# Kernel optimization log

Hardware: AMD Instinct MI355X
Metric: run time of the kernel (lower is better)

Reference implementation:

```python
import jax, jax.numpy as jnp
import numpy as np

B, L, D, H = 2, 2048, 1024, 16
DH = D // H  # 64
SIGMA = float(np.sqrt(DH))  # sigma=None, learnable_sigma=False -> sqrt(d_head)


def setup_inputs() -> dict:
    key = jax.random.key(0)
    ks = jax.random.split(key, 5)
    x = jax.random.normal(ks[0], (B, L, D), dtype=jnp.float32)
    # causal visibility mask (1 = visible, 0 = masked), [B,1,L,L]
    mask = jnp.broadcast_to(jnp.tril(jnp.ones((L, L), jnp.int32))[None, None], (B, 1, L, L))
    scale = 0.02
    W_q = jax.random.normal(ks[1], (D, D), dtype=jnp.float32) * scale
    W_k = jax.random.normal(ks[2], (D, D), dtype=jnp.float32) * scale
    W_v = jax.random.normal(ks[3], (D, D), dtype=jnp.float32) * scale
    W_o = jax.random.normal(ks[4], (D, D), dtype=jnp.float32) * scale
    return {"x": x, "mask": mask, "W_q": W_q, "W_k": W_k, "W_v": W_v, "W_o": W_o}


def _split_heads(t):
    # [B,L,D] -> [B,H,L,DH]
    b, l, _ = t.shape
    return t.reshape(b, l, H, DH).transpose(0, 2, 1, 3)


def reference(x, mask, W_q, W_k, W_v, W_o):
    # nn.Linear(bias=False): y = x @ W.T
    Qh = _split_heads(x @ W_q.T)  # [B,H,L,DH]
    Kh = _split_heads(x @ W_k.T)
    Vh = _split_heads(x @ W_v.T)
    # RBF scores: -||q-k||^2 / (2 sigma^2)
    q_norm2 = jnp.sum(Qh * Qh, axis=-1, keepdims=True)          # [B,H,L,1]
    k_norm2 = jnp.sum(Kh * Kh, axis=-1)[..., None, :]            # [B,H,1,L]
    dot_qk = jnp.einsum('bhqd,bhkd->bhqk', Qh, Kh)               # [B,H,L,L]
    dist2 = q_norm2 + k_norm2 - 2.0 * dot_qk
    scores = -dist2 / (2.0 * SIGMA * SIGMA)
    scores = jnp.where(mask == 0, -jnp.inf, scores)
    attn = jax.nn.softmax(scores, axis=-1)
    Oh = jnp.einsum('bhqk,bhkd->bhqd', attn, Vh)                 # [B,H,L,DH]
    O = Oh.transpose(0, 2, 1, 3).reshape(B, L, D)
    return O @ W_o.T
```

## Files before the change

kernel.cpp:

```cpp
#include <hip/hip_runtime.h>

#define L_SEQ  2048
#define D_MODEL 1024
#define NH 16
#define DHEAD 64
#define BATCH 2

typedef __attribute__((ext_vector_type(8))) short bf16x8;
typedef __attribute__((ext_vector_type(4))) float f32x4;

__device__ inline ushort f2bf(float f) {
  unsigned int u = __builtin_bit_cast(unsigned int, f);
  return (ushort)((u + 0x7FFFu + ((u >> 16) & 1u)) >> 16);
}
__device__ inline float bf2f(ushort u) {
  return __builtin_bit_cast(float, (unsigned int)u << 16);
}

__device__ __forceinline__ void gload_lds16(const void* g, void* l) {
  __builtin_amdgcn_global_load_lds(
      (const __attribute__((address_space(1))) void*)g,
      (__attribute__((address_space(3))) void*)l, 16, 0, 0);
}

#define PROJ8 524288
#define WSZ8  131072
__global__ __launch_bounds__(256) void cvt_all(const float* __restrict__ x,
                                               const float* __restrict__ w0,
                                               const float* __restrict__ w1,
                                               const float* __restrict__ w2,
                                               const float* __restrict__ w3,
                                               ushort* __restrict__ xb,
                                               ushort* __restrict__ ob0,
                                               ushort* __restrict__ ob1,
                                               ushort* __restrict__ ob2,
                                               ushort* __restrict__ ob3) {
  const int gid = blockIdx.x * 256 + threadIdx.x;
  const float* in; ushort* out; int off;
  if (gid < PROJ8) { in = x; out = xb; off = gid; }
  else {
    const int j = gid - PROJ8;
    const int seg = j / WSZ8;
    off = j - seg * WSZ8;
    switch (seg) {
      case 0: in = w0; out = ob0; break;
      case 1: in = w1; out = ob1; break;
      case 2: in = w2; out = ob2; break;
      default: in = w3; out = ob3; break;
    }
  }
  const float4* p = (const float4*)in + (size_t)off * 2;
  const float4 a = p[0], b = p[1];
  ushort4 lo, hi;
  lo.x = f2bf(a.x); lo.y = f2bf(a.y); lo.z = f2bf(a.z); lo.w = f2bf(a.w);
  hi.x = f2bf(b.x); hi.y = f2bf(b.y); hi.z = f2bf(b.z); hi.w = f2bf(b.w);
  ((ushort4*)out)[(size_t)off * 2] = lo;
  ((ushort4*)out)[(size_t)off * 2 + 1] = hi;
}

__global__ __launch_bounds__(512, 2) void gemm8p(const ushort* __restrict__ A,
    const ushort* __restrict__ W0, const ushort* __restrict__ W1,
    const ushort* __restrict__ W2, ushort* __restrict__ Qb,
    ushort* __restrict__ Kb, ushort* __restrict__ Vtb) {
  __shared__ ushort As[2][2][128][64];
  __shared__ ushort Bs[2][2][128][64];
  const int tid = threadIdx.x;
  const int wid = tid >> 6, l = tid & 63, lr = l & 15, lg = l >> 4;
  const int wr = wid >> 2, wc = wid & 3;

  const int bid = blockIdx.x;
  const int swz = (bid & 7) * 24 + (bid >> 3);
  const int mt = swz / 12, nt_ = swz % 12;
  const int m0g = mt * 256;
  const ushort* W = (nt_ < 4) ? W0 : (nt_ < 8) ? W1 : W2;
  ushort* outQK = (nt_ < 4) ? Qb : Kb;
  const int mode2 = (nt_ >= 8);
  const int ncol0 = (nt_ & 3) * 256;

  const int srow = tid >> 3;
  const int schunk = (tid & 7) ^ (srow & 7);
  const ushort* Ag = A + (size_t)(m0g + srow) * D_MODEL + schunk * 8;
  const ushort* Wg = W + (size_t)(ncol0 + srow) * D_MODEL + schunk * 8;
  ushort* AsL = &As[0][0][0][0] + tid * 8;
  ushort* BsL = &Bs[0][0][0][0] + tid * 8;

#define STG_A(sl, h, T2)                                                        \
  {                                                                             \
    gload_lds16(Ag + (size_t)((h) * 128) * D_MODEL + (T2) * 64,                 \
                AsL + (sl) * 16384 + (h) * 8192);                               \
    gload_lds16(Ag + (size_t)((h) * 128 + 64) * D_MODEL + (T2) * 64,            \
                AsL + (sl) * 16384 + (h) * 8192 + 4096);                        \
  }
#define STG_B(sl, h, T2)                                                        \
  {                                                                             \
    gload_lds16(Wg + (size_t)((h) * 128) * D_MODEL + (T2) * 64,                 \
                BsL + (sl) * 16384 + (h) * 8192);                               \
    gload_lds16(Wg + (size_t)((h) * 128 + 64) * D_MODEL + (T2) * 64,            \
                BsL + (sl) * 16384 + (h) * 8192 + 4096);                        \
  }

  STG_A(0, 0, 0); STG_A(0, 1, 0); STG_B(0, 0, 0); STG_B(0, 1, 0);

  f32x4 acc[8][4] = {};
  bf16x8 bfr[4][2];
  const int NT = D_MODEL / 64;

#define PHASE(q)                                                                \
  {                                                                             \
    bf16x8 af[2][2];                                                            \
    _Pragma("unroll") for (int m2 = 0; m2 < 2; ++m2)                            \
      _Pragma("unroll") for (int kk = 0; kk < 2; ++kk)                          \
        af[m2][kk] = *(const bf16x8*)&As[s][wr][((q) * 2 + m2) * 16 + lr]       \
                                           [((kk * 4 + lg) ^ (lr & 7)) * 8];    \
    if (T + 1 < NT) {                                                           \
      if ((q) == 1)      { STG_A(s ^ 1, 1, T + 1); }                            \
      else if ((q) == 2) { STG_B(s ^ 1, 0, T + 1); }                            \
      else               { STG_B(s ^ 1, 1, T + 1); }                            \
    }                                                                           \
    __builtin_amdgcn_s_barrier();                                               \
    __builtin_amdgcn_s_setprio(1);                                              \
    _Pragma("unroll") for (int m2 = 0; m2 < 2; ++m2)                            \
      _Pragma("unroll") for (int kk = 0; kk < 2; ++kk)                          \
        _Pragma("unroll") for (int n = 0; n < 4; ++n)                           \
          acc[(q) * 2 + m2][n] = __builtin_amdgcn_mfma_f32_16x16x32_bf16(       \
              af[m2][kk], bfr[n][kk], acc[(q) * 2 + m2][n], 0, 0, 0);           \
    __builtin_amdgcn_s_setprio(0);                                              \
    __builtin_amdgcn_s_barrier();                                               \
  }

  for (int T = 0; T < NT; ++T) {
    const int s = T & 1;
    {
      if (T + 1 < NT) {
        STG_A(s ^ 1, 0, T + 1);
        asm volatile("s_waitcnt vmcnt(2)" ::: "memory");
      } else {
        asm volatile("s_waitcnt vmcnt(0)" ::: "memory");
      }
      __builtin_amdgcn_s_barrier();
#pragma unroll
      for (int n = 0; n < 4; ++n)
#pragma unroll
        for (int kk = 0; kk < 2; ++kk)
          bfr[n][kk] = *(const bf16x8*)&Bs[s][wc >> 1][(wc & 1) * 64 + n * 16 + lr]
                                          [((kk * 4 + lg) ^ (lr & 7)) * 8];
      bf16x8 af[2][2];
#pragma unroll
      for (int m2 = 0; m2 < 2; ++m2)
#pragma unroll
        for (int kk = 0; kk < 2; ++kk)
          af[m2][kk] = *(const bf16x8*)&As[s][wr][m2 * 16 + lr]
                                          [((kk * 4 + lg) ^ (lr & 7)) * 8];
      __builtin_amdgcn_s_setprio(1);
#pragma unroll
      for (int m2 = 0; m2 < 2; ++m2)
#pragma unroll
        for (int kk = 0; kk < 2; ++kk)
#pragma unroll
          for (int n = 0; n < 4; ++n)
            acc[m2][n] = __builtin_amdgcn_mfma_f32_16x16x32_bf16(
                af[m2][kk], bfr[n][kk], acc[m2][n], 0, 0, 0);
      __builtin_amdgcn_s_setprio(0);
      __builtin_amdgcn_s_barrier();
    }
    PHASE(1)
    PHASE(2)
    PHASE(3)
  }
#undef PHASE
#undef STG_A
#undef STG_B

  const int h = (nt_ & 3) * 4 + wc;
  if (!mode2) {
#pragma unroll
    for (int m = 0; m < 8; ++m)
#pragma unroll
      for (int r = 0; r < 4; ++r) {
        const int grow = m0g + wr * 128 + m * 16 + lg * 4 + r;
        const int b = grow >> 11, ll = grow & (L_SEQ - 1);
        ushort* dst = outQK + ((size_t)(b * NH + h) * L_SEQ + ll) * DHEAD;
#pragma unroll
        for (int n = 0; n < 4; ++n) dst[n * 16 + lr] = f2bf(acc[m][n][r]);
      }
  } else {
#pragma unroll
    for (int m = 0; m < 8; ++m) {
      const int grow0 = m0g + wr * 128 + m * 16 + lg * 4;
      const int b = grow0 >> 11, ll = grow0 & (L_SEQ - 1);
#pragma unroll
      for (int n = 0; n < 4; ++n) {
        ushort4 v;
        v.x = f2bf(acc[m][n][0]); v.y = f2bf(acc[m][n][1]);
        v.z = f2bf(acc[m][n][2]); v.w = f2bf(acc[m][n][3]);
        *(ushort4*)(Vtb + ((size_t)(b * NH + h) * DHEAD + n * 16 + lr) * L_SEQ + ll) = v;
      }
    }
  }
}

__global__ __launch_bounds__(256) void gemm128(const ushort* __restrict__ A,
    const ushort* __restrict__ W0, float* __restrict__ of) {
  __shared__ ushort As[2][128][32];
  __shared__ ushort Bs[2][128][32];
  const int tid = threadIdx.x;
  const int w = tid >> 6, l = tid & 63, lr = l & 15, lg = l >> 4;
  const int wr = w >> 1, wc = w & 1;

  const int cpx = gridDim.x >> 3;
  const int swz = (blockIdx.x & 7) * cpx + (blockIdx.x >> 3);
  const int ntile = swz % 8;
  const int m0 = (swz / 8) * 128;
  const int n0 = ntile * 128;

  const int srow = tid >> 2;
  const int skc_sw = (tid & 3) ^ (srow & 3);
  const ushort* Ag = A + (size_t)(m0 + srow) * D_MODEL + skc_sw * 8;
  const ushort* Wg = W0 + (size_t)(n0 + srow) * D_MODEL + skc_sw * 8;

#define STAGE(buf, k0)                                                      \
  {                                                                         \
    gload_lds16(Ag + (k0), &As[buf][0][0] + tid * 8);                       \
    gload_lds16(Ag + (size_t)64 * D_MODEL + (k0), &As[buf][0][0] + 2048 + tid * 8); \
    gload_lds16(Wg + (k0), &Bs[buf][0][0] + tid * 8);                       \
    gload_lds16(Wg + (size_t)64 * D_MODEL + (k0), &Bs[buf][0][0] + 2048 + tid * 8); \
  }

  STAGE(0, 0);

  f32x4 acc[4][4] = {};
  const int NT = D_MODEL / 32;
  for (int t = 0; t < NT; ++t) {
    const int cur = t & 1;
    if (t + 1 < NT) {
      STAGE(cur ^ 1, (t + 1) * 32);
      asm volatile("s_waitcnt vmcnt(4)" ::: "memory");
    } else {
      asm volatile("s_waitcnt vmcnt(0)" ::: "memory");
    }
    __builtin_amdgcn_s_barrier();

    bf16x8 af[4], bfv[4];
#pragma unroll
    for (int i = 0; i < 4; ++i)
      af[i] = *(const bf16x8*)&As[cur][wr * 64 + i * 16 + lr][(lg ^ (lr & 3)) * 8];
#pragma unroll
    for (int j = 0; j < 4; ++j)
      bfv[j] = *(const bf16x8*)&Bs[cur][wc * 64 + j * 16 + lr][(lg ^ (lr & 3)) * 8];
#pragma unroll
    for (int i = 0; i < 4; ++i)
#pragma unroll
      for (int j = 0; j < 4; ++j)
        acc[i][j] = __builtin_amdgcn_mfma_f32_16x16x32_bf16(af[i], bfv[j], acc[i][j], 0, 0, 0);
    __builtin_amdgcn_s_barrier();
  }
#undef STAGE

#pragma unroll
  for (int i = 0; i < 4; ++i)
#pragma unroll
    for (int r = 0; r < 4; ++r) {
      const int m = m0 + wr * 64 + i * 16 + lg * 4 + r;
#pragma unroll
      for (int j = 0; j < 4; ++j)
        of[(size_t)m * D_MODEL + n0 + wc * 64 + j * 16 + lr] = acc[i][j][r];
    }
}

__global__ __launch_bounds__(256) void kn_bf16(const ushort* __restrict__ K,
                                               float* __restrict__ Kn) {
  const int i = blockIdx.x * 256 + threadIdx.x;
  const ushort4* p = (const ushort4*)(K + (size_t)i * DHEAD);
  float s = 0.f;
#pragma unroll
  for (int j = 0; j < 16; ++j) {
    const ushort4 v = p[j];
    const float a = bf2f(v.x), b = bf2f(v.y), c = bf2f(v.z), d = bf2f(v.w);
    s += a * a + b * b + c * c + d * d;
  }
  Kn[i] = s * 0.0078125f;
}

__global__ __launch_bounds__(256, 3) void attn_mfma4(const ushort* __restrict__ Q,
                                                     const ushort* __restrict__ K,
                                                     const ushort* __restrict__ Vt,
                                                     const float* __restrict__ Kexp,
                                                     ushort* __restrict__ Ob) {
  const int blk = blockIdx.x;
  const int qb = 31 - (blk >> 5);
  const int bh = blk & 31;
  const int tid = threadIdx.x;
  const int w = tid >> 6, l = tid & 63, lr = l & 15, lg = l >> 4;
  const int q0w = qb * 64 + w * 16;
  const int nt = qb + 1;

  __shared__ ushort Ks[2][64][64];
  __shared__ ushort Vs[2][64][64];
  __shared__ ushort P[4][16][70];

  const size_t ho = (size_t)bh * L_SEQ * DHEAD;
  const ushort* Qh = Q + ho;
  const ushort* Kh = K + ho;
  const ushort* Vh = Vt + ho;
  const float* KeB = Kexp + (size_t)bh * L_SEQ;

  const bf16x8 qf0 = *(const bf16x8*)(Qh + (size_t)(q0w + lr) * DHEAD + lg * 8);
  const bf16x8 qf1 = *(const bf16x8*)(Qh + (size_t)(q0w + lr) * DHEAD + 32 + lg * 8);

  const int srow = tid >> 3;
  const int scs = (tid & 7) ^ (srow & 7);
  const ushort* Kg = Kh + (size_t)srow * DHEAD + scs * 8;
  const ushort* Vg = Vh + (size_t)srow * L_SEQ + scs * 8;
  const ushort* Kg2 = Kg + (size_t)32 * DHEAD;
  const ushort* Vg2 = Vg + (size_t)32 * L_SEQ;

#define STAGE_KV(buf, kb)                                                 \
  {                                                                       \
    gload_lds16(Kg + (size_t)(kb) * DHEAD, &Ks[buf][0][0] + tid * 8);     \
    gload_lds16(Kg2 + (size_t)(kb) * DHEAD, &Ks[buf][32][0] + tid * 8);   \
    gload_lds16(Vg + (kb), &Vs[buf][0][0] + tid * 8);                     \
    gload_lds16(Vg2 + (kb), &Vs[buf][32][0] + tid * 8);                   \
  }

  float keC[4], keN[4] = {0.f, 0.f, 0.f, 0.f};
#pragma unroll
  for (int nf = 0; nf < 4; ++nf) keC[nf] = KeB[nf * 16 + lr];
  STAGE_KV(0, 0);

  f32x4 oacc[4] = {};
  f32x4 lsacc = {};
  bf16x8 ones;
#pragma unroll
  for (int i = 0; i < 8; ++i) ones[i] = (short)0x3F80;

  for (int t = 0; t < nt; ++t) {
    const int cur = t & 1;
    if (t + 1 < nt) {
#pragma unroll
      for (int nf = 0; nf < 4; ++nf) keN[nf] = KeB[(t + 1) * 64 + nf * 16 + lr];
      asm volatile("" ::: "memory");
      STAGE_KV(cur ^ 1, (size_t)(t + 1) * 64);
      asm volatile("s_waitcnt vmcnt(4)" ::: "memory");
    } else {
      asm volatile("s_waitcnt vmcnt(0)" ::: "memory");
    }
    __builtin_amdgcn_s_barrier();

    const int kbase = t * 64;
    const bool maskT = (t == qb);

    __builtin_amdgcn_s_setprio(1);
#pragma unroll
    for (int nf = 0; nf < 4; ++nf) {
      const int row = nf * 16 + lr;
      const bf16x8 kf0 = *(const bf16x8*)&Ks[cur][row][((lg) ^ (lr & 7)) * 8];
      const bf16x8 kf1 = *(const bf16x8*)&Ks[cur][row][((4 + lg) ^ (lr & 7)) * 8];
      f32x4 s = {0.f, 0.f, 0.f, 0.f};
      s = __builtin_amdgcn_mfma_f32_16x16x32_bf16(qf0, kf0, s, 0, 0, 0);
      s = __builtin_amdgcn_mfma_f32_16x16x32_bf16(qf1, kf1, s, 0, 0, 0);
      const int key = kbase + row;
      const float keh = keC[nf];
#pragma unroll
      for (int r = 0; r < 4; ++r) {
        float p = __expf(fmaf(s[r], 0.015625f, -keh));
        if (maskT && key > q0w + lg * 4 + r) p = 0.f;
        P[w][lg * 4 + r][nf * 16 + lr] = f2bf(p);
      }
    }
    const bf16x8 p0 = *(const bf16x8*)&P[w][lr][lg * 8];
    const bf16x8 p1 = *(const bf16x8*)&P[w][lr][32 + lg * 8];
    lsacc = __builtin_amdgcn_mfma_f32_16x16x32_bf16(p0, ones, lsacc, 0, 0, 0);
    lsacc = __builtin_amdgcn_mfma_f32_16x16x32_bf16(p1, ones, lsacc, 0, 0, 0);
#pragma unroll
    for (int nf = 0; nf < 4; ++nf) {
      const int row = nf * 16 + lr;
      const bf16x8 vf0 = *(const bf16x8*)&Vs[cur][row][((lg) ^ (lr & 7)) * 8];
      const bf16x8 vf1 = *(const bf16x8*)&Vs[cur][row][((4 + lg) ^ (lr & 7)) * 8];
      oacc[nf] = __builtin_amdgcn_mfma_f32_16x16x32_bf16(p0, vf0, oacc[nf], 0, 0, 0);
      oacc[nf] = __builtin_amdgcn_mfma_f32_16x16x32_bf16(p1, vf1, oacc[nf], 0, 0, 0);
    }
    __builtin_amdgcn_s_setprio(0);
    __builtin_amdgcn_s_barrier();
#pragma unroll
    for (int nf = 0; nf < 4; ++nf) keC[nf] = keN[nf];
  }
#undef STAGE_KV

  const int b = bh >> 4, h = bh & 15;
#pragma unroll
  for (int r = 0; r < 4; ++r) {
    const float inv = 1.0f / lsacc[r];
    const int q = q0w + lg * 4 + r;
#pragma unroll
    for (int nf = 0; nf < 4; ++nf)
      Ob[((size_t)(b * L_SEQ + q)) * D_MODEL + h * DHEAD + nf * 16 + lr] =
          f2bf(oacc[nf][r] * inv);
  }
}

extern "C" void kernel_launch(void* const* d_in, const int* in_sizes, int n_in,
                              void* d_out, int out_size, void* d_ws, size_t ws_size,
                              hipStream_t stream) {
  const float* x  = (const float*)d_in[0];
  const float* Wq = (const float*)d_in[2];
  const float* Wk = (const float*)d_in[3];
  const float* Wv = (const float*)d_in[4];
  const float* Wo = (const float*)d_in[5];

  const size_t PROJ = (size_t)BATCH * L_SEQ * D_MODEL;
  const size_t WSZ  = (size_t)D_MODEL * D_MODEL;
  ushort* xb  = (ushort*)d_ws;
  ushort* Wqb = xb + PROJ;
  ushort* Wkb = Wqb + WSZ;
  ushort* Wvb = Wkb + WSZ;
  ushort* Wob = Wvb + WSZ;
  ushort* Qb  = Wob + WSZ;
  ushort* Kb  = Qb + PROJ;
  ushort* Vtb = Kb + PROJ;
  ushort* Obf = Vtb + PROJ;
  float*  Kn  = (float*)(Obf + PROJ);

  cvt_all<<<(PROJ8 + 4 * WSZ8) / 256, 256, 0, stream>>>(x, Wq, Wk, Wv, Wo,
                                                        xb, Wqb, Wkb, Wvb, Wob);
  gemm8p<<<192, 512, 0, stream>>>(xb, Wqb, Wkb, Wvb, Qb, Kb, Vtb);
  kn_bf16<<<BATCH * NH * L_SEQ / 256, 256, 0, stream>>>(Kb, Kn);
  attn_mfma4<<<BATCH * NH * (L_SEQ / 64), 256, 0, stream>>>(Qb, Kb, Vtb, Kn, Obf);
  gemm128<<<256, 256, 0, stream>>>(Obf, Wob, (float*)d_out);
}
```

Before: 123.7 us.

## Restructure projection GEMM prefetch schedule with fewer barriers per K-step

Reworks the software pipeline of the bf16 projection GEMM. Each K-step now starts with one full vmcnt(0) wait and a barrier. All A-tile prefetches for the next stage are issued up front and all B-tile prefetches after the first MFMA phase, replacing the old four-phase interleaving with two barriers per phase. The aim is to cut barrier and scheduling overhead. In exchange, waiting for all outstanding loads at the top of every step may reduce how much global-to-LDS traffic overlaps with MFMA work.

```diff
diff --git a/kernel.cpp b/kernel.cpp
--- a/kernel.cpp
+++ b/kernel.cpp
@@ -105,19 +105,13 @@
   bf16x8 bfr[4][2];
   const int NT = D_MODEL / 64;
 
-#define PHASE(q)                                                                \
+#define PHASE_MFMA(q)                                                           \
   {                                                                             \
     bf16x8 af[2][2];                                                            \
     _Pragma("unroll") for (int m2 = 0; m2 < 2; ++m2)                            \
       _Pragma("unroll") for (int kk = 0; kk < 2; ++kk)                          \
         af[m2][kk] = *(const bf16x8*)&As[s][wr][((q) * 2 + m2) * 16 + lr]       \
                                            [((kk * 4 + lg) ^ (lr & 7)) * 8];    \
-    if (T + 1 < NT) {                                                           \
-      if ((q) == 1)      { STG_A(s ^ 1, 1, T + 1); }                            \
-      else if ((q) == 2) { STG_B(s ^ 1, 0, T + 1); }                            \
-      else               { STG_B(s ^ 1, 1, T + 1); }                            \
-    }                                                                           \
-    __builtin_amdgcn_s_barrier();                                               \
     __builtin_amdgcn_s_setprio(1);                                              \
     _Pragma("unroll") for (int m2 = 0; m2 < 2; ++m2)                            \
       _Pragma("unroll") for (int kk = 0; kk < 2; ++kk)                          \
@@ -125,49 +119,29 @@
           acc[(q) * 2 + m2][n] = __builtin_amdgcn_mfma_f32_16x16x32_bf16(       \
               af[m2][kk], bfr[n][kk], acc[(q) * 2 + m2][n], 0, 0, 0);           \
     __builtin_amdgcn_s_setprio(0);                                              \
-    __builtin_amdgcn_s_barrier();                                               \
   }
 
   for (int T = 0; T < NT; ++T) {
     const int s = T & 1;
-    {
-      if (T + 1 < NT) {
-        STG_A(s ^ 1, 0, T + 1);
-        asm volatile("s_waitcnt vmcnt(2)" ::: "memory");
-      } else {
-        asm volatile("s_waitcnt vmcnt(0)" ::: "memory");
-      }
-      __builtin_amdgcn_s_barrier();
-#pragma unroll
-      for (int n = 0; n < 4; ++n)
-#pragma unroll
-        for (int kk = 0; kk < 2; ++kk)
-          bfr[n][kk] = *(const bf16x8*)&Bs[s][wc >> 1][(wc & 1) * 64 + n * 16 + lr]
-                                          [((kk * 4 + lg) ^ (lr & 7)) * 8];
-      bf16x8 af[2][2];
-#pragma unroll
-      for (int m2 = 0; m2 < 2; ++m2)
-#pragma unroll
-        for (int kk = 0; kk < 2; ++kk)
-          af[m2][kk] = *(const bf16x8*)&As[s][wr][m2 * 16 + lr]
-                                          [((kk * 4 + lg) ^ (lr & 7)) * 8];
-      __builtin_amdgcn_s_setprio(1);
-#pragma unroll
-      for (int m2 = 0; m2 < 2; ++m2)
-#pragma unroll
-        for (int kk = 0; kk < 2; ++kk)
-#pragma unroll
-          for (int n = 0; n < 4; ++n)
-            acc[m2][n] = __builtin_amdgcn_mfma_f32_16x16x32_bf16(
-                af[m2][kk], bfr[n][kk], acc[m2][n], 0, 0, 0);
-      __builtin_amdgcn_s_setprio(0);
-      __builtin_amdgcn_s_barrier();
-    }
-    PHASE(1)
-    PHASE(2)
-    PHASE(3)
-  }
-#undef PHASE
+    asm volatile("s_waitcnt vmcnt(0)" ::: "memory");
+    __builtin_amdgcn_s_barrier();
+    if (T + 1 < NT) { STG_A(s ^ 1, 0, T + 1); STG_A(s ^ 1, 1, T + 1); }
+#pragma unroll
+    for (int n = 0; n < 4; ++n)
+#pragma unroll
+      for (int kk = 0; kk < 2; ++kk)
+        bfr[n][kk] = *(const bf16x8*)&Bs[s][wc >> 1][(wc & 1) * 64 + n * 16 + lr]
+                                        [((kk * 4 + lg) ^ (lr & 7)) * 8];
+    PHASE_MFMA(0)
+    __builtin_amdgcn_s_barrier();
+    if (T + 1 < NT) { STG_B(s ^ 1, 0, T + 1); STG_B(s ^ 1, 1, T + 1); }
+    PHASE_MFMA(1)
+    __builtin_amdgcn_s_barrier();
+    PHASE_MFMA(2)
+    __builtin_amdgcn_s_barrier();
+    PHASE_MFMA(3)
+  }
+#undef PHASE_MFMA
 #undef STG_A
 #undef STG_B
 
```

After: 129.9 us. 5.0% more time.
